# Performance work log

Hardware: AMD Instinct MI355X
Metric: run time of the kernel (lower is better)

The kernel has to match this reference:

```python
import jax, jax.numpy as jnp
import numpy as np

EMBED = 3072
NQ = 32
NKV = 8
HD = EMBED // NQ  # 96
GROUPS = NQ // NKV  # 4
ROPE_BASE = 10000.0


def apply_rope(t, positions):
    # t: [b, h, s, d]; positions: [s] int
    d = t.shape[-1]
    inv_freq = 1.0 / (ROPE_BASE ** (jnp.arange(0, d, 2, dtype=jnp.float32) / d))  # [d/2]
    ang = positions.astype(jnp.float32)[:, None] * inv_freq[None, :]  # [s, d/2]
    cos = jnp.cos(ang)[None, None]  # [1,1,s,d/2]
    sin = jnp.sin(ang)[None, None]
    t1, t2 = t[..., : d // 2], t[..., d // 2 :]
    return jnp.concatenate([t1 * cos - t2 * sin, t2 * cos + t1 * sin], axis=-1)


def setup_inputs() -> dict:
    key = jax.random.key(0)
    k1, k2, k3 = jax.random.split(key, 3)
    b, s = 2, 2048
    x = jax.random.normal(k1, (b, s, EMBED), dtype=jnp.float32)
    positions = jnp.arange(s, dtype=jnp.int32)
    mask = jnp.triu(jnp.ones((s, s), dtype=bool), k=1)  # True = masked (causal)
    qkv_size = NQ * HD + 2 * NKV * HD  # 4608
    W_qkv = jax.random.normal(k2, (qkv_size, EMBED), dtype=jnp.float32) * (EMBED ** -0.5)
    W_o = jax.random.normal(k3, (EMBED, EMBED), dtype=jnp.float32) * (EMBED ** -0.5)
    return {"x": x, "positions": positions, "mask": mask, "W_qkv": W_qkv, "W_o": W_o}


def reference(x, positions, mask, W_qkv, W_o):
    b, s, _ = x.shape
    scaling = HD ** -0.5
    qkv = x @ W_qkv.T  # [b, s, 4608]
    q_size, kv_size = NQ * HD, NKV * HD
    q = qkv[..., :q_size].reshape(b, s, NQ, HD).transpose(0, 2, 1, 3)          # [b,NQ,s,d]
    k = qkv[..., q_size : q_size + kv_size].reshape(b, s, NKV, HD).transpose(0, 2, 1, 3)
    v = qkv[..., q_size + kv_size :].reshape(b, s, NKV, HD).transpose(0, 2, 1, 3)
    q = apply_rope(q, positions)
    k = apply_rope(k, positions)
    q = q.reshape(b, NKV, GROUPS, s, HD)
    scores = jnp.einsum("bkgsd,bktd->bkgst", q, k) * scaling  # [b,NKV,G,s,s]
    scores = jnp.where(mask[None, None, None], -jnp.inf, scores)
    attn = jax.nn.softmax(scores, axis=-1)
    out = jnp.einsum("bkgst,bktd->bkgsd", attn, v)
    out = out.reshape(b, NQ, s, HD).transpose(0, 2, 1, 3).reshape(b, s, NQ * HD)
    return out @ W_o.T
```

## Files before the change

kernel.cpp:

```cpp
#include <hip/hip_runtime.h>
#include <cstdint>

typedef unsigned short u16;
typedef unsigned int u32;
typedef __attribute__((ext_vector_type(4))) float f32x4;
typedef __attribute__((ext_vector_type(8))) __bf16 bf16x8;
typedef __attribute__((ext_vector_type(8))) unsigned short u16x8;
typedef __attribute__((ext_vector_type(4))) unsigned int u32x4;

#define S_LEN 2048
#define BATCH 2
#define NQH 32
#define NKVH 8
#define HD 96
#define EMB 3072
#define QKVN 4608
#define KOFF 3072
#define VOFF 3840

__device__ __forceinline__ u16 f2b(float f) {
    u32 u = __float_as_uint(f);
    u32 r = (u + 0x7fffu + ((u >> 16) & 1u)) >> 16;
    return (u16)r;
}
__device__ __forceinline__ float b2f(u16 h) { return __uint_as_float(((u32)h) << 16); }
__device__ __forceinline__ u32 pk2(float a, float b) {
    return (u32)f2b(a) | ((u32)f2b(b) << 16);
}

__global__ __launch_bounds__(256) void conv_f2b(const float* __restrict__ in,
                                                u16* __restrict__ outp, int n8) {
    const int i = blockIdx.x * 256 + threadIdx.x;
    if (i >= n8) return;
    const f32x4* q = (const f32x4*)(in + (size_t)i * 8);
    const f32x4 a = q[0], b = q[1];
    u16x8 t;
#pragma unroll
    for (int j = 0; j < 4; ++j) {
        t[j] = f2b(a[j]);
        t[j + 4] = f2b(b[j]);
    }
    *(u16x8*)(outp + (size_t)i * 8) = t;
}

template <bool F32>
__device__ __forceinline__ bf16x8 load_frag8(const void* base, size_t elem) {
    if constexpr (F32) {
        const f32x4* q = (const f32x4*)((const float*)base + elem);
        const f32x4 a = q[0], b = q[1];
        u16x8 t;
#pragma unroll
        for (int i = 0; i < 4; ++i) {
            t[i] = f2b(a[i]);
            t[i + 4] = f2b(b[i]);
        }
        return __builtin_bit_cast(bf16x8, t);
    } else {
        return *(const bf16x8*)((const u16*)base + elem);
    }
}

template <bool AF32, bool BF32, bool OUTF32>
__global__ __launch_bounds__(256) void gqa_gemm_bt(const void* __restrict__ Ap,
                                                   const void* __restrict__ Bp,
                                                   void* __restrict__ Cp,
                                                   int M, int N, int K) {
    __shared__ __align__(16) u16 As[128 * 32];
    __shared__ __align__(16) u16 Bs[128 * 32];
    const int tid = threadIdx.x;
    const int wave = tid >> 6, lane = tid & 63;
    const int bm = blockIdx.y * 128, bn = blockIdx.x * 128;
    const int wm = (wave >> 1) * 64, wn = (wave & 1) * 64;
    const int lrow = lane & 15, lk = (lane >> 4) * 8;
    const int ra = tid >> 2, ca = (tid & 3) * 8;
    const int rb = (tid + 256) >> 2, cb = (tid & 3) * 8;
    f32x4 acc[4][4] = {};

    for (int k0 = 0; k0 < K; k0 += 32) {
        const bf16x8 a0 = load_frag8<AF32>(Ap, (size_t)(bm + ra) * K + k0 + ca);
        const bf16x8 a1 = load_frag8<AF32>(Ap, (size_t)(bm + rb) * K + k0 + cb);
        const bf16x8 b0 = load_frag8<BF32>(Bp, (size_t)(bn + ra) * K + k0 + ca);
        const bf16x8 b1 = load_frag8<BF32>(Bp, (size_t)(bn + rb) * K + k0 + cb);
        __syncthreads();
        *(bf16x8*)(As + ra * 32 + ca) = a0;
        *(bf16x8*)(As + rb * 32 + cb) = a1;
        *(bf16x8*)(Bs + ra * 32 + ca) = b0;
        *(bf16x8*)(Bs + rb * 32 + cb) = b1;
        __syncthreads();
        bf16x8 af[4], bfr[4];
#pragma unroll
        for (int mi = 0; mi < 4; ++mi)
            af[mi] = *(const bf16x8*)(As + (wm + mi * 16 + lrow) * 32 + lk);
#pragma unroll
        for (int ni = 0; ni < 4; ++ni)
            bfr[ni] = *(const bf16x8*)(Bs + (wn + ni * 16 + lrow) * 32 + lk);
#pragma unroll
        for (int mi = 0; mi < 4; ++mi)
#pragma unroll
            for (int ni = 0; ni < 4; ++ni)
                acc[mi][ni] = __builtin_amdgcn_mfma_f32_16x16x32_bf16(af[mi], bfr[ni],
                                                                      acc[mi][ni], 0, 0, 0);
    }
    const int orow = bm + wm + (lane >> 4) * 4;
    const int ocol = bn + wn + lrow;
#pragma unroll
    for (int mi = 0; mi < 4; ++mi)
#pragma unroll
        for (int ni = 0; ni < 4; ++ni)
#pragma unroll
            for (int r = 0; r < 4; ++r) {
                const size_t idx = (size_t)(orow + mi * 16 + r) * N + ocol + ni * 16;
                if constexpr (OUTF32)
                    ((float*)Cp)[idx] = acc[mi][ni][r];
                else
                    ((u16*)Cp)[idx] = f2b(acc[mi][ni][r]);
            }
}

__global__ __launch_bounds__(256) void gqa_rope(u16* __restrict__ qkv,
                                                const int* __restrict__ positions) {
    int i = blockIdx.x * 256 + threadIdx.x;
    const int pair = i % 48;
    int t = i / 48;
    const int head = t % (NQH + NKVH);
    const int bs = t / (NQH + NKVH);
    const int pos = positions[bs & (S_LEN - 1)];
    const size_t base = (size_t)bs * QKVN + (head < NQH ? head * HD : KOFF + (head - NQH) * HD);
    const float invf = __expf(-(float)(2 * pair) * (1.0f / 96.0f) * 9.210340371976184f);
    const float ang = (float)pos * invf;
    float sn, cs;
    __sincosf(ang, &sn, &cs);
    const float t1 = b2f(qkv[base + pair]);
    const float t2 = b2f(qkv[base + 48 + pair]);
    qkv[base + pair] = f2b(t1 * cs - t2 * sn);
    qkv[base + 48 + pair] = f2b(t2 * cs + t1 * sn);
}

__global__ __launch_bounds__(256) void gqa_attn3(const u16* __restrict__ qkv,
                                                 u16* __restrict__ out) {
    __shared__ __align__(16) u16 Ks[64 * 96];
    __shared__ __align__(16) u16 Vt[96 * 72];

    const int tid = threadIdx.x;
    const int wave = tid >> 6, lane = tid & 63;
    const int lrow = lane & 15, lhi = lane >> 4;
    const int bx = blockIdx.x;
    const int qt32 = 63 - (bx >> 4);
    const int kvh = (bx >> 1) & 7, bb = bx & 1;
    const int qh = kvh * 4 + wave;
    const int srow0 = bb * S_LEN + qt32 * 32;
    const int kb_last = (qt32 * 32 + 31) >> 6;
    const float cl2 = 0.10206207261596575f * 1.4426950408889634f;

    bf16x8 bq[2][3];
#pragma unroll
    for (int qt = 0; qt < 2; ++qt)
#pragma unroll
        for (int kd = 0; kd < 3; ++kd)
            bq[qt][kd] = *(const bf16x8*)(qkv + (size_t)(srow0 + qt * 16 + lrow) * QKVN +
                                          qh * 96 + kd * 32 + lhi * 8);

    float m_s[2] = {-3e38f, -3e38f}, l_s[2] = {0.0f, 0.0f};
    f32x4 oacc[6][2] = {};

    const int s0 = lrow + ((lane & 16) ? 32 : 0);
    const int s1 = s0 + 16;
    const bool khi = (lane & 32) != 0;

    const size_t kvrow0 = (size_t)(bb * S_LEN) * QKVN;
    for (int kb = 0; kb <= kb_last; ++kb) {
        __syncthreads();
        const size_t kbase = kvrow0 + (size_t)(kb * 64) * QKVN + KOFF + kvh * 96;
        const size_t vbase = kvrow0 + (size_t)(kb * 64) * QKVN + VOFF + kvh * 96;
        for (int u = tid; u < 768; u += 256) {
            const int oct = u % 12, row = u / 12;
            *(u16x8*)(Ks + row * 96 + oct * 8) =
                *(const u16x8*)(qkv + kbase + (size_t)row * QKVN + oct * 8);
        }
        for (int u = tid; u < 768; u += 256) {
            const int d = u % 96, so8 = u / 96;
            u16x8 v8;
#pragma unroll
            for (int j = 0; j < 8; ++j) v8[j] = qkv[vbase + (size_t)(so8 * 8 + j) * QKVN + d];
            *(u16x8*)(Vt + d * 72 + so8 * 8) = v8;
        }
        __syncthreads();

        bf16x8 ka[4][3];
#pragma unroll
        for (int kt = 0; kt < 4; ++kt)
#pragma unroll
            for (int kd = 0; kd < 3; ++kd)
                ka[kt][kd] = *(const bf16x8*)(Ks + (kt * 16 + lrow) * 96 + kd * 32 + lhi * 8);

        const int qoff = qt32 * 32 - kb * 64;
        const bool lastkb = (kb == kb_last);
        u32 bp[2][2][4];

#pragma unroll
        for (int qt = 0; qt < 2; ++qt) {
            const int qrelmax = qoff + qt * 16 + 15;
            f32x4 sacc[4] = {};
#pragma unroll
            for (int kt = 0; kt < 4; ++kt) {
                if (lastkb && kt * 16 > qrelmax) continue;
#pragma unroll
                for (int kd = 0; kd < 3; ++kd)
                    sacc[kt] = __builtin_amdgcn_mfma_f32_16x16x32_bf16(ka[kt][kd], bq[qt][kd],
                                                                       sacc[kt], 0, 0, 0);
            }
            float p[4][4];
            float mx = -3e38f;
            if (lastkb) {
                const int qrel = qoff + qt * 16 + lrow;
#pragma unroll
                for (int kt = 0; kt < 4; ++kt)
#pragma unroll
                    for (int r = 0; r < 4; ++r) {
                        const bool live = (kt * 16 + lhi * 4 + r) <= qrel;
                        const float s = live ? sacc[kt][r] : -3e38f;
                        p[kt][r] = s;
                        mx = fmaxf(mx, s);
                    }
            } else {
#pragma unroll
                for (int kt = 0; kt < 4; ++kt)
#pragma unroll
                    for (int r = 0; r < 4; ++r) {
                        p[kt][r] = sacc[kt][r];
                        mx = fmaxf(mx, sacc[kt][r]);
                    }
            }
            mx = fmaxf(mx, __shfl_xor(mx, 16));
            mx = fmaxf(mx, __shfl_xor(mx, 32));
            const float mn = fmaxf(m_s[qt], mx);
            const float alpha = exp2f((m_s[qt] - mn) * cl2);
            m_s[qt] = mn;
            float rs = 0.0f;
#pragma unroll
            for (int kt = 0; kt < 4; ++kt)
#pragma unroll
                for (int r = 0; r < 4; ++r) {
                    const float pv = exp2f((p[kt][r] - mn) * cl2);
                    p[kt][r] = pv;
                    rs += pv;
                }
            rs += __shfl_xor(rs, 16);
            rs += __shfl_xor(rs, 32);
            l_s[qt] = l_s[qt] * alpha + rs;
#pragma unroll
            for (int dt = 0; dt < 6; ++dt)
#pragma unroll
                for (int r = 0; r < 4; ++r) oacc[dt][qt][r] *= alpha;
            u32 pk[4][2];
#pragma unroll
            for (int kt = 0; kt < 4; ++kt) {
                pk[kt][0] = pk2(p[kt][0], p[kt][1]);
                pk[kt][1] = pk2(p[kt][2], p[kt][3]);
            }
#pragma unroll
            for (int kk = 0; kk < 2; ++kk) {
                const u32 a0 = (u32)__shfl((int)pk[kk * 2][0], s0, 64);
                const u32 b0 = (u32)__shfl((int)pk[kk * 2 + 1][0], s0, 64);
                const u32 a1 = (u32)__shfl((int)pk[kk * 2][1], s0, 64);
                const u32 b1 = (u32)__shfl((int)pk[kk * 2 + 1][1], s0, 64);
                const u32 a2 = (u32)__shfl((int)pk[kk * 2][0], s1, 64);
                const u32 b2 = (u32)__shfl((int)pk[kk * 2 + 1][0], s1, 64);
                const u32 a3 = (u32)__shfl((int)pk[kk * 2][1], s1, 64);
                const u32 b3 = (u32)__shfl((int)pk[kk * 2 + 1][1], s1, 64);
                bp[qt][kk][0] = khi ? b0 : a0;
                bp[qt][kk][1] = khi ? b1 : a1;
                bp[qt][kk][2] = khi ? b2 : a2;
                bp[qt][kk][3] = khi ? b3 : a3;
            }
        }

#pragma unroll
        for (int dt = 0; dt < 6; ++dt) {
            bf16x8 va[2];
#pragma unroll
            for (int kk = 0; kk < 2; ++kk)
                va[kk] = *(const bf16x8*)(Vt + (dt * 16 + lrow) * 72 + kk * 32 + lhi * 8);
#pragma unroll
            for (int qt = 0; qt < 2; ++qt)
#pragma unroll
                for (int kk = 0; kk < 2; ++kk) {
                    const u32x4 bv = {bp[qt][kk][0], bp[qt][kk][1], bp[qt][kk][2], bp[qt][kk][3]};
                    oacc[dt][qt] = __builtin_amdgcn_mfma_f32_16x16x32_bf16(
                        va[kk], __builtin_bit_cast(bf16x8, bv), oacc[dt][qt], 0, 0, 0);
                }
        }
    }

    const size_t obase = (size_t)srow0 * EMB + qh * 96;
#pragma unroll
    for (int qt = 0; qt < 2; ++qt) {
        const float inv = 1.0f / l_s[qt];
        const size_t rbase = obase + (size_t)(qt * 16 + lrow) * EMB;
#pragma unroll
        for (int dt = 0; dt < 6; ++dt)
#pragma unroll
            for (int rp = 0; rp < 2; ++rp) {
                const u32 pair = pk2(oacc[dt][qt][2 * rp] * inv, oacc[dt][qt][2 * rp + 1] * inv);
                *(u32*)(out + rbase + dt * 16 + lhi * 4 + 2 * rp) = pair;
            }
    }
}

extern "C" void kernel_launch(void* const* d_in, const int* in_sizes, int n_in,
                              void* d_out, int out_size, void* d_ws, size_t ws_size,
                              hipStream_t stream) {
    const float* x = (const float*)d_in[0];
    const int* positions = (const int*)d_in[1];
    const float* W_qkv = (const float*)d_in[3];
    const float* W_o = (const float*)d_in[4];
    float* out = (float*)d_out;

    const int M = BATCH * S_LEN;
    const size_t QKV_E = (size_t)M * QKVN;
    const size_t ATT_E = (size_t)M * EMB;
    const size_t X_E = (size_t)M * EMB;
    const size_t WQ_E = (size_t)QKVN * EMB;
    const size_t WO_E = (size_t)EMB * EMB;

    u16* qkv_ws = (u16*)d_ws;
    u16* attn_ws = qkv_ws + QKV_E;
    u16* xb = attn_ws + ATT_E;
    u16* wqb = xb + X_E;
    u16* wob = wqb + WQ_E;
    const size_t need = (QKV_E + ATT_E + X_E + WQ_E + WO_E) * 2;

    if (ws_size >= need) {
        conv_f2b<<<(int)(X_E / 8 + 255) / 256, 256, 0, stream>>>(x, xb, (int)(X_E / 8));
        conv_f2b<<<(int)(WQ_E / 8 + 255) / 256, 256, 0, stream>>>(W_qkv, wqb, (int)(WQ_E / 8));
        conv_f2b<<<(int)(WO_E / 8 + 255) / 256, 256, 0, stream>>>(W_o, wob, (int)(WO_E / 8));
        gqa_gemm_bt<false, false, false>
            <<<dim3(QKVN / 128, M / 128), 256, 0, stream>>>(xb, wqb, qkv_ws, M, QKVN, EMB);
        gqa_rope<<<(BATCH * S_LEN * (NQH + NKVH) * 48) / 256, 256, 0, stream>>>(qkv_ws, positions);
        gqa_attn3<<<dim3(1024), 256, 0, stream>>>(qkv_ws, attn_ws);
        gqa_gemm_bt<false, false, true>
            <<<dim3(EMB / 128, M / 128), 256, 0, stream>>>(attn_ws, wob, out, M, EMB, EMB);
    } else {
        gqa_gemm_bt<true, true, false>
            <<<dim3(QKVN / 128, M / 128), 256, 0, stream>>>(x, W_qkv, qkv_ws, M, QKVN, EMB);
        gqa_rope<<<(BATCH * S_LEN * (NQH + NKVH) * 48) / 256, 256, 0, stream>>>(qkv_ws, positions);
        gqa_attn3<<<dim3(1024), 256, 0, stream>>>(qkv_ws, attn_ws);
        gqa_gemm_bt<false, true, true>
            <<<dim3(EMB / 128, M / 128), 256, 0, stream>>>(attn_ws, W_o, out, M, EMB, EMB);
    }
}
```

Before: 665.6 us.

## Use direct global-to-LDS loads, lazy softmax rescale, hardware bf16 pack, workspace reuse

The GEMM now loads bf16 tiles straight into LDS with global_load_lds for the bf16 operands, so tiles no longer pass through registers. Attention skips the online-softmax rescale unless the running max grows by more than a threshold, and float-to-bf16 packing uses the v_cvt_pk_bf16_f32 instruction. The workspace layout is rearranged: x is converted into the output buffer and the attention output aliases the weight buffer, which lowers the workspace the fast path needs. The aliasing assumes the converted W_qkv is dead by the time attention writes over it, and the lazy rescale trades exactness of the max for fewer multiplies.

```diff
diff --git a/kernel.cpp b/kernel.cpp
--- a/kernel.cpp
+++ b/kernel.cpp
@@ -24,8 +24,10 @@
     return (u16)r;
 }
 __device__ __forceinline__ float b2f(u16 h) { return __uint_as_float(((u32)h) << 16); }
-__device__ __forceinline__ u32 pk2(float a, float b) {
-    return (u32)f2b(a) | ((u32)f2b(b) << 16);
+__device__ __forceinline__ u32 cvtpk(float lo, float hi) {
+    u32 r;
+    asm("v_cvt_pk_bf16_f32 %0, %1, %2" : "=v"(r) : "v"(lo), "v"(hi));
+    return r;
 }
 
 __global__ __launch_bounds__(256) void conv_f2b(const float* __restrict__ in,
@@ -43,28 +45,29 @@
     *(u16x8*)(outp + (size_t)i * 8) = t;
 }
 
-template <bool F32>
-__device__ __forceinline__ bf16x8 load_frag8(const void* base, size_t elem) {
-    if constexpr (F32) {
-        const f32x4* q = (const f32x4*)((const float*)base + elem);
-        const f32x4 a = q[0], b = q[1];
-        u16x8 t;
-#pragma unroll
-        for (int i = 0; i < 4; ++i) {
-            t[i] = f2b(a[i]);
-            t[i + 4] = f2b(b[i]);
-        }
-        return __builtin_bit_cast(bf16x8, t);
-    } else {
-        return *(const bf16x8*)((const u16*)base + elem);
-    }
+typedef __attribute__((address_space(1))) const uint32_t gas_u32;
+typedef __attribute__((address_space(3))) uint32_t las_u32;
+__device__ __forceinline__ void gld_lds16(const u16* g, u16* l) {
+    __builtin_amdgcn_global_load_lds((gas_u32*)g, (las_u32*)l, 16, 0, 0);
+}
+
+__device__ __forceinline__ bf16x8 cvt_frag8_f32(const void* base, size_t elem) {
+    const f32x4* q = (const f32x4*)((const float*)base + elem);
+    const f32x4 a = q[0], b = q[1];
+    u16x8 t;
+#pragma unroll
+    for (int i = 0; i < 4; ++i) {
+        t[i] = f2b(a[i]);
+        t[i + 4] = f2b(b[i]);
+    }
+    return __builtin_bit_cast(bf16x8, t);
 }
 
 template <bool AF32, bool BF32, bool OUTF32>
-__global__ __launch_bounds__(256) void gqa_gemm_bt(const void* __restrict__ Ap,
-                                                   const void* __restrict__ Bp,
-                                                   void* __restrict__ Cp,
-                                                   int M, int N, int K) {
+__global__ __launch_bounds__(256) void gemm_bt(const void* __restrict__ Ap,
+                                               const void* __restrict__ Bp,
+                                               void* __restrict__ Cp,
+                                               int M, int N, int K) {
     __shared__ __align__(16) u16 As[128 * 32];
     __shared__ __align__(16) u16 Bs[128 * 32];
     const int tid = threadIdx.x;
@@ -73,19 +76,44 @@
     const int wm = (wave >> 1) * 64, wn = (wave & 1) * 64;
     const int lrow = lane & 15, lk = (lane >> 4) * 8;
     const int ra = tid >> 2, ca = (tid & 3) * 8;
-    const int rb = (tid + 256) >> 2, cb = (tid & 3) * 8;
+
+    const u16* gA0 = (const u16*)Ap + (size_t)(bm + ra) * K + ca;
+    const u16* gA1 = (const u16*)Ap + (size_t)(bm + ra + 64) * K + ca;
+    const u16* gB0 = (const u16*)Bp + (size_t)(bn + ra) * K + ca;
+    const u16* gB1 = (const u16*)Bp + (size_t)(bn + ra + 64) * K + ca;
+    u16* lA0 = As + (tid & 192) * 8;
+    u16* lA1 = lA0 + 2048;
+    u16* lB0 = Bs + (tid & 192) * 8;
+    u16* lB1 = lB0 + 2048;
+
     f32x4 acc[4][4] = {};
-
     for (int k0 = 0; k0 < K; k0 += 32) {
-        const bf16x8 a0 = load_frag8<AF32>(Ap, (size_t)(bm + ra) * K + k0 + ca);
-        const bf16x8 a1 = load_frag8<AF32>(Ap, (size_t)(bm + rb) * K + k0 + cb);
-        const bf16x8 b0 = load_frag8<BF32>(Bp, (size_t)(bn + ra) * K + k0 + ca);
-        const bf16x8 b1 = load_frag8<BF32>(Bp, (size_t)(bn + rb) * K + k0 + cb);
+        bf16x8 a0, a1, b0, b1;
+        if constexpr (AF32) {
+            a0 = cvt_frag8_f32(Ap, (size_t)(bm + ra) * K + k0 + ca);
+            a1 = cvt_frag8_f32(Ap, (size_t)(bm + ra + 64) * K + k0 + ca);
+        }
+        if constexpr (BF32) {
+            b0 = cvt_frag8_f32(Bp, (size_t)(bn + ra) * K + k0 + ca);
+            b1 = cvt_frag8_f32(Bp, (size_t)(bn + ra + 64) * K + k0 + ca);
+        }
         __syncthreads();
-        *(bf16x8*)(As + ra * 32 + ca) = a0;
-        *(bf16x8*)(As + rb * 32 + cb) = a1;
-        *(bf16x8*)(Bs + ra * 32 + ca) = b0;
-        *(bf16x8*)(Bs + rb * 32 + cb) = b1;
+        if constexpr (!AF32) {
+            gld_lds16(gA0 + k0, lA0);
+            gld_lds16(gA1 + k0, lA1);
+        }
+        if constexpr (!BF32) {
+            gld_lds16(gB0 + k0, lB0);
+            gld_lds16(gB1 + k0, lB1);
+        }
+        if constexpr (AF32) {
+            *(bf16x8*)(As + ra * 32 + ca) = a0;
+            *(bf16x8*)(As + (ra + 64) * 32 + ca) = a1;
+        }
+        if constexpr (BF32) {
+            *(bf16x8*)(Bs + ra * 32 + ca) = b0;
+            *(bf16x8*)(Bs + (ra + 64) * 32 + ca) = b1;
+        }
         __syncthreads();
         bf16x8 af[4], bfr[4];
 #pragma unroll
@@ -233,9 +261,18 @@
             }
             mx = fmaxf(mx, __shfl_xor(mx, 16));
             mx = fmaxf(mx, __shfl_xor(mx, 32));
-            const float mn = fmaxf(m_s[qt], mx);
-            const float alpha = exp2f((m_s[qt] - mn) * cl2);
-            m_s[qt] = mn;
+            float mn = m_s[qt];
+            if (!__all(mx - mn <= 20.0f)) {
+                const float mnew = fmaxf(mn, mx);
+                const float alpha = exp2f((mn - mnew) * cl2);
+                m_s[qt] = mnew;
+                mn = mnew;
+                l_s[qt] *= alpha;
+#pragma unroll
+                for (int dt = 0; dt < 6; ++dt)
+#pragma unroll
+                    for (int r = 0; r < 4; ++r) oacc[dt][qt][r] *= alpha;
+            }
             float rs = 0.0f;
 #pragma unroll
             for (int kt = 0; kt < 4; ++kt)
@@ -247,16 +284,12 @@
                 }
             rs += __shfl_xor(rs, 16);
             rs += __shfl_xor(rs, 32);
-            l_s[qt] = l_s[qt] * alpha + rs;
-#pragma unroll
-            for (int dt = 0; dt < 6; ++dt)
-#pragma unroll
-                for (int r = 0; r < 4; ++r) oacc[dt][qt][r] *= alpha;
+            l_s[qt] += rs;
             u32 pk[4][2];
 #pragma unroll
             for (int kt = 0; kt < 4; ++kt) {
-                pk[kt][0] = pk2(p[kt][0], p[kt][1]);
-                pk[kt][1] = pk2(p[kt][2], p[kt][3]);
+                pk[kt][0] = cvtpk(p[kt][0], p[kt][1]);
+                pk[kt][1] = cvtpk(p[kt][2], p[kt][3]);
             }
 #pragma unroll
             for (int kk = 0; kk < 2; ++kk) {
@@ -301,7 +334,7 @@
         for (int dt = 0; dt < 6; ++dt)
 #pragma unroll
             for (int rp = 0; rp < 2; ++rp) {
-                const u32 pair = pk2(oacc[dt][qt][2 * rp] * inv, oacc[dt][qt][2 * rp + 1] * inv);
+                const u32 pair = cvtpk(oacc[dt][qt][2 * rp] * inv, oacc[dt][qt][2 * rp + 1] * inv);
                 *(u32*)(out + rbase + dt * 16 + lhi * 4 + 2 * rp) = pair;
             }
     }
@@ -323,29 +356,44 @@
     const size_t WQ_E = (size_t)QKVN * EMB;
     const size_t WO_E = (size_t)EMB * EMB;
 
-    u16* qkv_ws = (u16*)d_ws;
-    u16* attn_ws = qkv_ws + QKV_E;
-    u16* xb = attn_ws + ATT_E;
-    u16* wqb = xb + X_E;
-    u16* wob = wqb + WQ_E;
-    const size_t need = (QKV_E + ATT_E + X_E + WQ_E + WO_E) * 2;
-
-    if (ws_size >= need) {
-        conv_f2b<<<(int)(X_E / 8 + 255) / 256, 256, 0, stream>>>(x, xb, (int)(X_E / 8));
-        conv_f2b<<<(int)(WQ_E / 8 + 255) / 256, 256, 0, stream>>>(W_qkv, wqb, (int)(WQ_E / 8));
-        conv_f2b<<<(int)(WO_E / 8 + 255) / 256, 256, 0, stream>>>(W_o, wob, (int)(WO_E / 8));
-        gqa_gemm_bt<false, false, false>
-            <<<dim3(QKVN / 128, M / 128), 256, 0, stream>>>(xb, wqb, qkv_ws, M, QKVN, EMB);
-        gqa_rope<<<(BATCH * S_LEN * (NQH + NKVH) * 48) / 256, 256, 0, stream>>>(qkv_ws, positions);
-        gqa_attn3<<<dim3(1024), 256, 0, stream>>>(qkv_ws, attn_ws);
-        gqa_gemm_bt<false, false, true>
+    u16* xb = (u16*)d_out;
+    conv_f2b<<<(int)(X_E / 8 / 256), 256, 0, stream>>>(x, xb, (int)(X_E / 8));
+
+    const size_t needA = (WQ_E + WO_E + QKV_E) * 2;
+    const size_t needB = (WQ_E + QKV_E) * 2;
+
+    if (ws_size >= needA) {
+        u16* wqb = (u16*)d_ws;
+        u16* wob = wqb + WQ_E;
+        u16* qkv = wob + WO_E;
+        u16* attn_ws = (u16*)d_ws;
+        conv_f2b<<<(int)(WQ_E / 8 / 256), 256, 0, stream>>>(W_qkv, wqb, (int)(WQ_E / 8));
+        conv_f2b<<<(int)(WO_E / 8 / 256), 256, 0, stream>>>(W_o, wob, (int)(WO_E / 8));
+        gemm_bt<false, false, false>
+            <<<dim3(QKVN / 128, M / 128), 256, 0, stream>>>(xb, wqb, qkv, M, QKVN, EMB);
+        gqa_rope<<<(BATCH * S_LEN * (NQH + NKVH) * 48) / 256, 256, 0, stream>>>(qkv, positions);
+        gqa_attn3<<<dim3(1024), 256, 0, stream>>>(qkv, attn_ws);
+        gemm_bt<false, false, true>
             <<<dim3(EMB / 128, M / 128), 256, 0, stream>>>(attn_ws, wob, out, M, EMB, EMB);
+    } else if (ws_size >= needB) {
+        u16* wqb = (u16*)d_ws;
+        u16* qkv = wqb + WQ_E;
+        u16* attn_ws = (u16*)d_ws;
+        conv_f2b<<<(int)(WQ_E / 8 / 256), 256, 0, stream>>>(W_qkv, wqb, (int)(WQ_E / 8));
+        gemm_bt<false, false, false>
+            <<<dim3(QKVN / 128, M / 128), 256, 0, stream>>>(xb, wqb, qkv, M, QKVN, EMB);
+        gqa_rope<<<(BATCH * S_LEN * (NQH + NKVH) * 48) / 256, 256, 0, stream>>>(qkv, positions);
+        gqa_attn3<<<dim3(1024), 256, 0, stream>>>(qkv, attn_ws);
+        gemm_bt<false, true, true>
+            <<<dim3(EMB / 128, M / 128), 256, 0, stream>>>(attn_ws, W_o, out, M, EMB, EMB);
     } else {
-        gqa_gemm_bt<true, true, false>
-            <<<dim3(QKVN / 128, M / 128), 256, 0, stream>>>(x, W_qkv, qkv_ws, M, QKVN, EMB);
-        gqa_rope<<<(BATCH * S_LEN * (NQH + NKVH) * 48) / 256, 256, 0, stream>>>(qkv_ws, positions);
-        gqa_attn3<<<dim3(1024), 256, 0, stream>>>(qkv_ws, attn_ws);
-        gqa_gemm_bt<false, true, true>
+        u16* qkv = (u16*)d_ws;
+        u16* attn_ws = qkv + QKV_E;
+        gemm_bt<false, true, false>
+            <<<dim3(QKVN / 128, M / 128), 256, 0, stream>>>(xb, W_qkv, qkv, M, QKVN, EMB);
+        gqa_rope<<<(BATCH * S_LEN * (NQH + NKVH) * 48) / 256, 256, 0, stream>>>(qkv, positions);
+        gqa_attn3<<<dim3(1024), 256, 0, stream>>>(qkv, attn_ws);
+        gemm_bt<false, true, true>
             <<<dim3(EMB / 128, M / 128), 256, 0, stream>>>(attn_ws, W_o, out, M, EMB, EMB);
     }
 }
```

Result: faster. 647.0 us (-2.8%).
